# Performance work log

Measured on AMD Instinct MI355X. Metric: run time of the kernel, lower is better.

## Reference

```python
import jax, jax.numpy as jnp
import numpy as np

NUM_GRAPHS = 512
LEAKY_SLOPE = 0.01


def _gconv(x, src, dst, w, W_root, W_rel, b_rel):
    # PyG GraphConv: out = lin_rel(sum_j w_ij * x_j) + lin_root(x)
    msg = x[src] * w[:, None]                       # [E, d] gather + scale
    agg = jax.ops.segment_sum(msg, dst, num_segments=x.shape[0])  # scatter-add
    return agg @ W_rel + b_rel + x @ W_root


def setup_inputs() -> dict:
    key = jax.random.key(0)
    ks = jax.random.split(key, 12)
    N, E, D, H, C = 100000, 1250000, 64, 64, 8
    x_embeddings = jax.random.normal(ks[0], (N, D), dtype=jnp.float32)
    edge_index = jax.random.randint(ks[1], (2, E), 0, N, dtype=jnp.int64)
    weights = jax.random.uniform(ks[2], (E,), dtype=jnp.float32)
    batch = jnp.sort(jax.random.randint(ks[3], (N,), 0, NUM_GRAPHS, dtype=jnp.int64))
    s1 = 1.0 / np.sqrt(D)
    s2 = 1.0 / np.sqrt(H)
    W1_root = jax.random.uniform(ks[4], (D, H), jnp.float32, -s1, s1)
    W1_rel = jax.random.uniform(ks[5], (D, H), jnp.float32, -s1, s1)
    b1 = jax.random.uniform(ks[6], (H,), jnp.float32, -s1, s1)
    W2_root = jax.random.uniform(ks[7], (H, H), jnp.float32, -s2, s2)
    W2_rel = jax.random.uniform(ks[8], (H, H), jnp.float32, -s2, s2)
    b2 = jax.random.uniform(ks[9], (H,), jnp.float32, -s2, s2)
    Wl_root = jax.random.uniform(ks[10], (H, C), jnp.float32, -s2, s2)
    bl = jax.random.uniform(ks[11], (C,), jnp.float32, -s2, s2)
    return {"x_embeddings": x_embeddings, "edge_index": edge_index,
            "weights": weights, "batch": batch,
            "W1_root": W1_root, "W1_rel": W1_rel, "b1": b1,
            "W2_root": W2_root, "W2_rel": W2_rel, "b2": b2,
            "Wl_root": Wl_root, "bl": bl}


def reference(x_embeddings, edge_index, weights, batch,
              W1_root, W1_rel, b1, W2_root, W2_rel, b2, Wl_root, bl):
    src, dst = edge_index[0], edge_index[1]
    x = _gconv(x_embeddings, src, dst, weights, W1_root, W1_rel, b1)
    x = jax.nn.leaky_relu(x, LEAKY_SLOPE)
    x = _gconv(x, src, dst, weights, W2_root, W2_rel, b2)
    x = jax.nn.leaky_relu(x, LEAKY_SLOPE)
    # global_mean_pool over graph ids
    summed = jax.ops.segment_sum(x, batch, num_segments=NUM_GRAPHS)
    counts = jax.ops.segment_sum(jnp.ones((x.shape[0],), x.dtype), batch,
                                 num_segments=NUM_GRAPHS)
    pooled = summed / jnp.maximum(counts, 1.0)[:, None]
    # final GraphConv applied with no edges: agg = 0 -> W_root x + b_rel
    out = pooled @ Wl_root + bl
    return out
```

## Files before the change

kernel.cpp:

```cpp
#include <hip/hip_runtime.h>

#define LEAKY_SLOPE 0.01f
#define NUM_GRAPHS 512
#define TILE 4096
#define NB_MAX 512
#define POOL_SPAN 8

typedef __attribute__((ext_vector_type(8))) short short8;
typedef __attribute__((ext_vector_type(4))) float f32x4;

static __device__ __forceinline__ unsigned short f2bf(float f) {
    unsigned u = __float_as_uint(f);
    u += 0x7FFFu + ((u >> 16) & 1u);
    return (unsigned short)(u >> 16);
}
static __device__ __forceinline__ float bf2f(unsigned short h) {
    return __uint_as_float(((unsigned)h) << 16);
}

static __device__ __forceinline__ int wave_incl_scan(int v, int lane) {
#pragma unroll
    for (int off = 1; off < 64; off <<= 1) {
        int t = __shfl_up(v, off, 64);
        if (lane >= off) v += t;
    }
    return v;
}

__global__ __launch_bounds__(256)
void mega_prep(const int* __restrict__ dst, int* __restrict__ bucketCnt, int E,
               int NB, int histBlocks,
               const float* __restrict__ x, unsigned short* __restrict__ xB,
               int xElems , int xBlocks,
               const float* __restrict__ W1rel, const float* __restrict__ W1root,
               const float* __restrict__ W2rel, const float* __restrict__ W2root,
               unsigned short* __restrict__ Bt1, unsigned short* __restrict__ Bt2) {
    const int bid = blockIdx.x;
    if (bid < histBlocks) {
        __shared__ int h[NB_MAX];
        for (int t = threadIdx.x; t < NB_MAX; t += 256) h[t] = 0;
        __syncthreads();
        const int base = bid * TILE;
#pragma unroll
        for (int i = 0; i < TILE / 256; ++i) {
            int e = base + i * 256 + threadIdx.x;
            if (e < E) atomicAdd(&h[dst[e] >> 8], 1);
        }
        __syncthreads();
        for (int t = threadIdx.x; t < NB; t += 256)
            if (h[t]) atomicAdd(&bucketCnt[t], h[t]);
    } else if (bid < histBlocks + xBlocks) {
        int i = (bid - histBlocks) * 256 + threadIdx.x;
        if (i < xElems) {
            float4 f = ((const float4*)x)[i];
            ushort4 o = make_ushort4(f2bf(f.x), f2bf(f.y), f2bf(f.z), f2bf(f.w));
            ((ushort4*)xB)[i] = o;
        }
    } else {
        int b2 = bid - histBlocks - xBlocks;
        for (int idx = b2 * 2048 + threadIdx.x; idx < (b2 + 1) * 2048; idx += 256) {
            int which = idx >> 13;
            int j = idx & 8191;
            int n = j >> 7, k = j & 127;
            const float* Wr = which ? W2rel : W1rel;
            const float* Wo = which ? W2root : W1root;
            float v = (k < 64) ? Wr[k * 64 + n] : Wo[(k - 64) * 64 + n];
            (which ? Bt2 : Bt1)[j] = f2bf(v);
        }
    }
}

__global__ __launch_bounds__(512)
void bscan_kernel(const int* __restrict__ bucketCnt, int* __restrict__ bucketBase,
                  int* __restrict__ cursor, int* __restrict__ rowStart,
                  float* __restrict__ pooled, int N, int E, int NB) {
    __shared__ int ws[8];
    const int t = threadIdx.x, lane = t & 63, wid = t >> 6;
    int v = (t < NB) ? bucketCnt[t] : 0;
    int s = wave_incl_scan(v, lane);
    if (lane == 63) ws[wid] = s;
    __syncthreads();
    int add = 0;
    for (int i = 0; i < wid; ++i) add += ws[i];
    if (t < NB) {
        int excl = s + add - v;
        bucketBase[t] = excl;
        cursor[t] = excl;
    }
    if (t == 0) rowStart[N] = E;
    float4 z = make_float4(0.f, 0.f, 0.f, 0.f);
#pragma unroll
    for (int i = 0; i < 16; ++i)
        ((float4*)pooled)[t * 16 + i] = z;
}

__global__ __launch_bounds__(256)
void p1b_partition(const int* __restrict__ src, const int* __restrict__ dst,
                   const float* __restrict__ w, int* __restrict__ cursor,
                   int2* __restrict__ tmp, int E, int NB) {
    __shared__ int h[NB_MAX];
    __shared__ int cur[NB_MAX];
    __shared__ int lstart[NB_MAX];
    __shared__ int gbase[NB_MAX];
    __shared__ int ws[4];
    __shared__ int2 pay[TILE];
    __shared__ unsigned short bk[TILE];

    for (int t = threadIdx.x; t < NB_MAX; t += 256) h[t] = 0;
    __syncthreads();

    const int base = blockIdx.x * TILE;
    int   myb[TILE / 256];
    int   myp[TILE / 256];
    float myw[TILE / 256];
#pragma unroll
    for (int i = 0; i < TILE / 256; ++i) {
        int e = base + i * 256 + threadIdx.x;
        if (e < E) {
            int d = dst[e];
            myb[i] = d >> 8;
            myp[i] = src[e] | ((d & 255) << 20);
            myw[i] = w[e];
            atomicAdd(&h[myb[i]], 1);
        } else {
            myb[i] = -1;
        }
    }
    __syncthreads();

    {
        const int t = threadIdx.x, lane = t & 63, wid = t >> 6;
        int a = h[2 * t], b = h[2 * t + 1];
        int s = wave_incl_scan(a + b, lane);
        if (lane == 63) ws[wid] = s;
        __syncthreads();
        int add = 0;
        for (int i = 0; i < wid; ++i) add += ws[i];
        int excl = s + add - (a + b);
        lstart[2 * t] = excl;
        lstart[2 * t + 1] = excl + a;
        cur[2 * t] = excl;
        cur[2 * t + 1] = excl + a;
    }
    __syncthreads();

#pragma unroll
    for (int i = 0; i < TILE / 256; ++i) {
        if (myb[i] >= 0) {
            int p = atomicAdd(&cur[myb[i]], 1);
            pay[p] = make_int2(myp[i], __float_as_int(myw[i]));
            bk[p] = (unsigned short)myb[i];
        }
    }
    __syncthreads();

    for (int t = threadIdx.x; t < NB; t += 256) {
        int c = h[t];
        if (c) gbase[t] = atomicAdd(&cursor[t], c);
    }
    __syncthreads();

    const int total = min(TILE, E - base);
    for (int s2 = threadIdx.x; s2 < total; s2 += 256) {
        int b2 = bk[s2];
        tmp[gbase[b2] + s2 - lstart[b2]] = pay[s2];
    }
}

__global__ __launch_bounds__(256)
void p2_build(const int2* __restrict__ tmp, const int* __restrict__ bucketBase,
              int* __restrict__ rowStart, int2* __restrict__ edata,
              int N, int E, int NB) {
    const int b = blockIdx.x;
    const int s = bucketBase[b];
    const int e2 = (b + 1 < NB) ? bucketBase[b + 1] : E;
    __shared__ int h[256];
    __shared__ int cur[256];
    __shared__ int ws[4];
    h[threadIdx.x] = 0;
    __syncthreads();
    for (int j = s + threadIdx.x; j < e2; j += 256) {
        int dl = (tmp[j].x >> 20) & 255;
        atomicAdd(&h[dl], 1);
    }
    __syncthreads();
    const int t = threadIdx.x, lane = t & 63, wid = t >> 6;
    int v = h[t];
    int sc = wave_incl_scan(v, lane);
    if (lane == 63) ws[wid] = sc;
    __syncthreads();
    int add = 0;
    for (int i = 0; i < wid; ++i) add += ws[i];
    int excl = sc + add - v;
    const int node = b * 256 + t;
    if (node < N) rowStart[node] = s + excl;
    cur[t] = excl;
    __syncthreads();
    for (int j = s + threadIdx.x; j < e2; j += 256) {
        int2 v2 = tmp[j];
        int dl = (v2.x >> 20) & 255;
        int p = atomicAdd(&cur[dl], 1);
        edata[s + p] = make_int2(v2.x & 0x1FFFF, v2.y);
    }
}

__global__ __launch_bounds__(256)
void gather_kernel(const unsigned short* __restrict__ xB, const int* __restrict__ rowStart,
                   const int2* __restrict__ edata, unsigned short* __restrict__ aggB, int N) {
    const int node = blockIdx.x * 4 + (threadIdx.x >> 6);
    if (node >= N) return;
    const int lane = threadIdx.x & 63;
    const int grp  = lane >> 4;
    const int f4   = (lane & 15) * 4;
    const int s = rowStart[node];
    const int e = rowStart[node + 1];

    float a0 = 0.f, a1 = 0.f, a2 = 0.f, a3 = 0.f;
    for (int j = s; j < e; j += 16) {
        int   idx[4];
        int2  ed[4];
#pragma unroll
        for (int u = 0; u < 4; ++u) {
            int ii = j + u * 4 + grp;
            idx[u] = (ii < e) ? ii : s;
            ed[u] = edata[idx[u]];
        }
        ushort4 r[4];
#pragma unroll
        for (int u = 0; u < 4; ++u)
            r[u] = *(const ushort4*)(xB + (size_t)ed[u].x * 64 + f4);
#pragma unroll
        for (int u = 0; u < 4; ++u) {
            int ii = j + u * 4 + grp;
            float wv = (ii < e) ? __int_as_float(ed[u].y) : 0.0f;
            a0 += bf2f(r[u].x) * wv;  a1 += bf2f(r[u].y) * wv;
            a2 += bf2f(r[u].z) * wv;  a3 += bf2f(r[u].w) * wv;
        }
    }
    a0 += __shfl_xor(a0, 16, 64);  a1 += __shfl_xor(a1, 16, 64);
    a2 += __shfl_xor(a2, 16, 64);  a3 += __shfl_xor(a3, 16, 64);
    a0 += __shfl_xor(a0, 32, 64);  a1 += __shfl_xor(a1, 32, 64);
    a2 += __shfl_xor(a2, 32, 64);  a3 += __shfl_xor(a3, 32, 64);
    if (grp == 0) {
        ushort4 o = make_ushort4(f2bf(a0), f2bf(a1), f2bf(a2), f2bf(a3));
        *(ushort4*)(aggB + (size_t)node * 64 + f4) = o;
    }
}

__global__ __launch_bounds__(256)
void transform_store(const unsigned short* __restrict__ aggB,
                     const unsigned short* __restrict__ rootB,
                     const unsigned short* __restrict__ Bt,
                     const float* __restrict__ bias,
                     unsigned short* __restrict__ xoutB, int N) {
    const int wave = threadIdx.x >> 6;
    const int lane = threadIdx.x & 63;
    const int quad = lane >> 4;
    const int l16  = lane & 15;
    const int m0   = blockIdx.x * 128 + wave * 32;

    short8 bf[4][4];
#pragma unroll
    for (int t = 0; t < 4; ++t)
#pragma unroll
        for (int k = 0; k < 4; ++k)
            bf[t][k] = *(const short8*)(Bt + (t * 16 + l16) * 128 + k * 32 + quad * 8);

    f32x4 acc[2][4];
#pragma unroll
    for (int s = 0; s < 2; ++s)
#pragma unroll
        for (int t = 0; t < 4; ++t)
            acc[s][t] = (f32x4){0.f, 0.f, 0.f, 0.f};

#pragma unroll
    for (int s = 0; s < 2; ++s) {
        int row = m0 + s * 16 + l16;
        int rowc = row < N ? row : N - 1;
        const unsigned short* arow = aggB  + (size_t)rowc * 64;
        const unsigned short* xrow = rootB + (size_t)rowc * 64;
        short8 af[4];
        af[0] = *(const short8*)(arow + quad * 8);
        af[1] = *(const short8*)(arow + 32 + quad * 8);
        af[2] = *(const short8*)(xrow + quad * 8);
        af[3] = *(const short8*)(xrow + 32 + quad * 8);
#pragma unroll
        for (int t = 0; t < 4; ++t)
#pragma unroll
            for (int k = 0; k < 4; ++k)
                acc[s][t] = __builtin_amdgcn_mfma_f32_16x16x32_bf16(bf[t][k], af[k],
                                                                    acc[s][t], 0, 0, 0);
    }

#pragma unroll
    for (int s = 0; s < 2; ++s) {
        const int node = m0 + s * 16 + l16;
        if (node < N) {
#pragma unroll
            for (int t = 0; t < 4; ++t) {
                const float4 bb = *(const float4*)(bias + t * 16 + quad * 4);
                float v0 = acc[s][t][0] + bb.x;
                float v1 = acc[s][t][1] + bb.y;
                float v2 = acc[s][t][2] + bb.z;
                float v3 = acc[s][t][3] + bb.w;
                v0 = (v0 > 0.f) ? v0 : LEAKY_SLOPE * v0;
                v1 = (v1 > 0.f) ? v1 : LEAKY_SLOPE * v1;
                v2 = (v2 > 0.f) ? v2 : LEAKY_SLOPE * v2;
                v3 = (v3 > 0.f) ? v3 : LEAKY_SLOPE * v3;
                ushort4 o = make_ushort4(f2bf(v0), f2bf(v1), f2bf(v2), f2bf(v3));
                *(ushort4*)(xoutB + (size_t)node * 64 + t * 16 + quad * 4) = o;
            }
        }
    }
}

__global__ __launch_bounds__(256)
void transform_pool(const unsigned short* __restrict__ aggB,
                    const unsigned short* __restrict__ rootB,
                    const unsigned short* __restrict__ Bt,
                    const float* __restrict__ bias,
                    const int* __restrict__ batch,
                    float* __restrict__ pooled, int N) {
    const int wave = threadIdx.x >> 6;
    const int lane = threadIdx.x & 63;
    const int quad = lane >> 4;
    const int l16  = lane & 15;
    const int m0   = blockIdx.x * 128 + wave * 32;

    __shared__ float lpool[POOL_SPAN * 64];
    const int gmin = batch[blockIdx.x * 128];
    for (int i = threadIdx.x; i < POOL_SPAN * 64; i += 256) lpool[i] = 0.f;

    short8 bf[4][4];
#pragma unroll
    for (int t = 0; t < 4; ++t)
#pragma unroll
        for (int k = 0; k < 4; ++k)
            bf[t][k] = *(const short8*)(Bt + (t * 16 + l16) * 128 + k * 32 + quad * 8);

    f32x4 acc[2][4];
#pragma unroll
    for (int s = 0; s < 2; ++s)
#pragma unroll
        for (int t = 0; t < 4; ++t)
            acc[s][t] = (f32x4){0.f, 0.f, 0.f, 0.f};

#pragma unroll
    for (int s = 0; s < 2; ++s) {
        int row = m0 + s * 16 + l16;
        int rowc = row < N ? row : N - 1;
        const unsigned short* arow = aggB  + (size_t)rowc * 64;
        const unsigned short* xrow = rootB + (size_t)rowc * 64;
        short8 af[4];
        af[0] = *(const short8*)(arow + quad * 8);
        af[1] = *(const short8*)(arow + 32 + quad * 8);
        af[2] = *(const short8*)(xrow + quad * 8);
        af[3] = *(const short8*)(xrow + 32 + quad * 8);
#pragma unroll
        for (int t = 0; t < 4; ++t)
#pragma unroll
            for (int k = 0; k < 4; ++k)
                acc[s][t] = __builtin_amdgcn_mfma_f32_16x16x32_bf16(af[k], bf[t][k],
                                                                    acc[s][t], 0, 0, 0);
    }

    __syncthreads();

#pragma unroll
    for (int s = 0; s < 2; ++s) {
#pragma unroll
        for (int t = 0; t < 4; ++t) {
            const int col = t * 16 + l16;
            const float b = bias[col];
            const int rowbase = m0 + s * 16 + quad * 4;
            float v[4]; int g[4]; int nv = 0;
#pragma unroll
            for (int r = 0; r < 4; ++r) {
                int row = rowbase + r;
                if (row < N) {
                    float a = acc[s][t][r] + b;
                    a = (a > 0.0f) ? a : LEAKY_SLOPE * a;
                    v[nv] = a;
                    g[nv] = batch[row];
                    ++nv;
                }
            }
            if (nv == 4 && g[0] == g[3]) {
                int gl = g[0] - gmin;
                float sum = v[0] + v[1] + v[2] + v[3];
                if (gl < POOL_SPAN) atomicAdd(&lpool[gl * 64 + col], sum);
                else                atomicAdd(&pooled[g[0] * 64 + col], sum);
            } else {
                for (int r = 0; r < nv; ++r) {
                    int gl = g[r] - gmin;
                    if (gl < POOL_SPAN) atomicAdd(&lpool[gl * 64 + col], v[r]);
                    else                atomicAdd(&pooled[g[r] * 64 + col], v[r]);
                }
            }
        }
    }

    __syncthreads();
    for (int i = threadIdx.x; i < POOL_SPAN * 64; i += 256) {
        float v = lpool[i];
        if (v != 0.0f)
            atomicAdd(&pooled[(gmin + (i >> 6)) * 64 + (i & 63)], v);
    }
}

__global__ __launch_bounds__(64)
void final_kernel(const float* __restrict__ pooled, const int* __restrict__ batch,
                  int N, const float* __restrict__ Wl, const float* __restrict__ bl,
                  float* __restrict__ out) {
    const int g = blockIdx.x;
    const int j = threadIdx.x;
    __shared__ float sp[64];
    __shared__ int scnt;
    if (j == 0) {
        int lo = 0, hi = N;
        while (lo < hi) { int mid = (lo + hi) >> 1; if (batch[mid] < g) lo = mid + 1; else hi = mid; }
        const int start = lo;
        hi = N;
        while (lo < hi) { int mid = (lo + hi) >> 1; if (batch[mid] < g + 1) lo = mid + 1; else hi = mid; }
        scnt = lo - start;
    }
    __syncthreads();
    const float c = fmaxf((float)scnt, 1.0f);
    sp[j] = pooled[g * 64 + j] / c;
    __syncthreads();
    if (j < 8) {
        float acc = bl[j];
#pragma unroll
        for (int k = 0; k < 64; ++k) acc += sp[k] * Wl[k * 8 + j];
        out[g * 8 + j] = acc;
    }
}

extern "C" void kernel_launch(void* const* d_in, const int* in_sizes, int n_in,
                              void* d_out, int out_size, void* d_ws, size_t ws_size,
                              hipStream_t stream) {
    const float* x      = (const float*)d_in[0];
    const int*   ei     = (const int*)  d_in[1];
    const float* w      = (const float*)d_in[2];
    const int*   batch  = (const int*)  d_in[3];
    const float* W1root = (const float*)d_in[4];
    const float* W1rel  = (const float*)d_in[5];
    const float* b1     = (const float*)d_in[6];
    const float* W2root = (const float*)d_in[7];
    const float* W2rel  = (const float*)d_in[8];
    const float* b2     = (const float*)d_in[9];
    const float* Wl     = (const float*)d_in[10];
    const float* bl     = (const float*)d_in[11];
    float* out = (float*)d_out;

    const int E = in_sizes[2];
    const int N = in_sizes[3];
    const int* src = ei;
    const int* dst = ei + E;
    const int NB = (N + 255) / 256;

    unsigned short* xB   = (unsigned short*)d_ws;
    unsigned short* aggB = xB   + (size_t)N * 64;
    unsigned short* x1B  = aggB + (size_t)N * 64;
    int2*  tmp      = (int2*)(x1B + (size_t)N * 64);
    int2*  edata    = tmp + E;
    unsigned short* Bt1 = (unsigned short*)(edata + E);
    unsigned short* Bt2 = Bt1 + 64 * 128;
    int*   rowStart = (int*)(Bt2 + 64 * 128);
    int*   bucketCnt  = rowStart + (N + 1);
    int*   bucketBase = bucketCnt + NB_MAX;
    int*   cursor     = bucketBase + NB_MAX;
    float* pooled   = (float*)(cursor + NB_MAX);

    const int histBlocks = (E + TILE - 1) / TILE;
    const int xElems = N * 16;
    const int xBlocks = (xElems + 255) / 256;

    hipMemsetAsync(bucketCnt, 0, NB_MAX * sizeof(int), stream);
    mega_prep<<<histBlocks + xBlocks + 8, 256, 0, stream>>>(
        dst, bucketCnt, E, NB, histBlocks,
        x, xB, xElems, xBlocks,
        W1rel, W1root, W2rel, W2root, Bt1, Bt2);
    bscan_kernel<<<1, 512, 0, stream>>>(bucketCnt, bucketBase, cursor, rowStart,
                                        pooled, N, E, NB);
    p1b_partition<<<histBlocks, 256, 0, stream>>>(src, dst, w, cursor, tmp, E, NB);
    p2_build<<<NB, 256, 0, stream>>>(tmp, bucketBase, rowStart, edata, N, E, NB);

    const int tBlocks = (N + 127) / 128;
    gather_kernel<<<(N + 3) / 4, 256, 0, stream>>>(xB, rowStart, edata, aggB, N);
    transform_store<<<tBlocks, 256, 0, stream>>>(aggB, xB, Bt1, b1, x1B, N);
    gather_kernel<<<(N + 3) / 4, 256, 0, stream>>>(x1B, rowStart, edata, aggB, N);
    transform_pool<<<tBlocks, 256, 0, stream>>>(aggB, x1B, Bt2, b2, batch, pooled, N);
    final_kernel<<<NUM_GRAPHS, 64, 0, stream>>>(pooled, batch, N, Wl, bl, out);
}
```

Baseline: 274.7 us.

## Fuse neighbor gather with MFMA transform into one kernel per layer

```diff
diff --git a/kernel.cpp b/kernel.cpp
--- a/kernel.cpp
+++ b/kernel.cpp
@@ -204,67 +204,76 @@
     }
 }
 
+template <int POOL>
 __global__ __launch_bounds__(256)
-void gather_kernel(const unsigned short* __restrict__ xB, const int* __restrict__ rowStart,
-                   const int2* __restrict__ edata, unsigned short* __restrict__ aggB, int N) {
-    const int node = blockIdx.x * 4 + (threadIdx.x >> 6);
-    if (node >= N) return;
+void fused_layer(const unsigned short* __restrict__ xin,
+                 const int* __restrict__ rowStart,
+                 const int2* __restrict__ edata,
+                 const unsigned short* __restrict__ Bt,
+                 const float* __restrict__ bias,
+                 unsigned short* __restrict__ xoutB,
+                 const int* __restrict__ batch,
+                 float* __restrict__ pooled, int N) {
     const int lane = threadIdx.x & 63;
+    const int wave = threadIdx.x >> 6;
     const int grp  = lane >> 4;
-    const int f4   = (lane & 15) * 4;
-    const int s = rowStart[node];
-    const int e = rowStart[node + 1];
-
-    float a0 = 0.f, a1 = 0.f, a2 = 0.f, a3 = 0.f;
-    for (int j = s; j < e; j += 16) {
-        int   idx[4];
-        int2  ed[4];
-#pragma unroll
-        for (int u = 0; u < 4; ++u) {
-            int ii = j + u * 4 + grp;
-            idx[u] = (ii < e) ? ii : s;
-            ed[u] = edata[idx[u]];
-        }
-        ushort4 r[4];
-#pragma unroll
-        for (int u = 0; u < 4; ++u)
-            r[u] = *(const ushort4*)(xB + (size_t)ed[u].x * 64 + f4);
-#pragma unroll
-        for (int u = 0; u < 4; ++u) {
-            int ii = j + u * 4 + grp;
-            float wv = (ii < e) ? __int_as_float(ed[u].y) : 0.0f;
-            a0 += bf2f(r[u].x) * wv;  a1 += bf2f(r[u].y) * wv;
-            a2 += bf2f(r[u].z) * wv;  a3 += bf2f(r[u].w) * wv;
-        }
-    }
-    a0 += __shfl_xor(a0, 16, 64);  a1 += __shfl_xor(a1, 16, 64);
-    a2 += __shfl_xor(a2, 16, 64);  a3 += __shfl_xor(a3, 16, 64);
-    a0 += __shfl_xor(a0, 32, 64);  a1 += __shfl_xor(a1, 32, 64);
-    a2 += __shfl_xor(a2, 32, 64);  a3 += __shfl_xor(a3, 32, 64);
-    if (grp == 0) {
-        ushort4 o = make_ushort4(f2bf(a0), f2bf(a1), f2bf(a2), f2bf(a3));
-        *(ushort4*)(aggB + (size_t)node * 64 + f4) = o;
-    }
-}
-
-__global__ __launch_bounds__(256)
-void transform_store(const unsigned short* __restrict__ aggB,
-                     const unsigned short* __restrict__ rootB,
-                     const unsigned short* __restrict__ Bt,
-                     const float* __restrict__ bias,
-                     unsigned short* __restrict__ xoutB, int N) {
-    const int wave = threadIdx.x >> 6;
-    const int lane = threadIdx.x & 63;
-    const int quad = lane >> 4;
     const int l16  = lane & 15;
-    const int m0   = blockIdx.x * 128 + wave * 32;
+    const int f4   = l16 * 4;
+    const int m0   = (int)blockIdx.x * 128 + wave * 32;
+
+    __shared__ __align__(16) unsigned short aggL[4][32][72];
+    __shared__ float lpool[POOL_SPAN * 64];
+
+    int gmin = 0;
+    if (POOL) {
+        int b0 = (int)blockIdx.x * 128;
+        gmin = batch[b0 < N ? b0 : N - 1];
+        for (int i = threadIdx.x; i < POOL_SPAN * 64; i += 256) lpool[i] = 0.f;
+    }
+
+    int rsv = 0;
+    if (lane <= 32) {
+        int rn = m0 + lane;
+        rsv = rowStart[rn < N ? rn : N];
+    }
+#pragma unroll 1
+    for (int i = 0; i < 32; ++i) {
+        const int s = __shfl(rsv, i, 64);
+        const int e = __shfl(rsv, i + 1, 64);
+        float a0 = 0.f, a1 = 0.f, a2 = 0.f, a3 = 0.f;
+        for (int j = s; j < e; j += 16) {
+            int2 ed[4];
+#pragma unroll
+            for (int u = 0; u < 4; ++u) {
+                int ii = j + u * 4 + grp;
+                ed[u] = edata[ii < e ? ii : s];
+            }
+            ushort4 r[4];
+#pragma unroll
+            for (int u = 0; u < 4; ++u)
+                r[u] = *(const ushort4*)(xin + (size_t)ed[u].x * 64 + f4);
+#pragma unroll
+            for (int u = 0; u < 4; ++u) {
+                float wv = (j + u * 4 + grp < e) ? __int_as_float(ed[u].y) : 0.0f;
+                a0 += bf2f(r[u].x) * wv;  a1 += bf2f(r[u].y) * wv;
+                a2 += bf2f(r[u].z) * wv;  a3 += bf2f(r[u].w) * wv;
+            }
+        }
+        a0 += __shfl_xor(a0, 16, 64);  a1 += __shfl_xor(a1, 16, 64);
+        a2 += __shfl_xor(a2, 16, 64);  a3 += __shfl_xor(a3, 16, 64);
+        a0 += __shfl_xor(a0, 32, 64);  a1 += __shfl_xor(a1, 32, 64);
+        a2 += __shfl_xor(a2, 32, 64);  a3 += __shfl_xor(a3, 32, 64);
+        if (grp == 0)
+            *(ushort4*)(&aggL[wave][i][f4]) =
+                make_ushort4(f2bf(a0), f2bf(a1), f2bf(a2), f2bf(a3));
+    }
 
     short8 bf[4][4];
 #pragma unroll
     for (int t = 0; t < 4; ++t)
 #pragma unroll
         for (int k = 0; k < 4; ++k)
-            bf[t][k] = *(const short8*)(Bt + (t * 16 + l16) * 128 + k * 32 + quad * 8);
+            bf[t][k] = *(const short8*)(Bt + (t * 16 + l16) * 128 + k * 32 + grp * 8);
 
     f32x4 acc[2][4];
 #pragma unroll
@@ -277,134 +286,87 @@
     for (int s = 0; s < 2; ++s) {
         int row = m0 + s * 16 + l16;
         int rowc = row < N ? row : N - 1;
-        const unsigned short* arow = aggB  + (size_t)rowc * 64;
-        const unsigned short* xrow = rootB + (size_t)rowc * 64;
+        const unsigned short* xrow = xin + (size_t)rowc * 64;
         short8 af[4];
-        af[0] = *(const short8*)(arow + quad * 8);
-        af[1] = *(const short8*)(arow + 32 + quad * 8);
-        af[2] = *(const short8*)(xrow + quad * 8);
-        af[3] = *(const short8*)(xrow + 32 + quad * 8);
+        af[0] = *(const short8*)(&aggL[wave][s * 16 + l16][grp * 8]);
+        af[1] = *(const short8*)(&aggL[wave][s * 16 + l16][32 + grp * 8]);
+        af[2] = *(const short8*)(xrow + grp * 8);
+        af[3] = *(const short8*)(xrow + 32 + grp * 8);
 #pragma unroll
         for (int t = 0; t < 4; ++t)
 #pragma unroll
-            for (int k = 0; k < 4; ++k)
-                acc[s][t] = __builtin_amdgcn_mfma_f32_16x16x32_bf16(bf[t][k], af[k],
-                                                                    acc[s][t], 0, 0, 0);
-    }
-
-#pragma unroll
-    for (int s = 0; s < 2; ++s) {
-        const int node = m0 + s * 16 + l16;
-        if (node < N) {
-#pragma unroll
-            for (int t = 0; t < 4; ++t) {
-                const float4 bb = *(const float4*)(bias + t * 16 + quad * 4);
-                float v0 = acc[s][t][0] + bb.x;
-                float v1 = acc[s][t][1] + bb.y;
-                float v2 = acc[s][t][2] + bb.z;
-                float v3 = acc[s][t][3] + bb.w;
-                v0 = (v0 > 0.f) ? v0 : LEAKY_SLOPE * v0;
-                v1 = (v1 > 0.f) ? v1 : LEAKY_SLOPE * v1;
-                v2 = (v2 > 0.f) ? v2 : LEAKY_SLOPE * v2;
-                v3 = (v3 > 0.f) ? v3 : LEAKY_SLOPE * v3;
-                ushort4 o = make_ushort4(f2bf(v0), f2bf(v1), f2bf(v2), f2bf(v3));
-                *(ushort4*)(xoutB + (size_t)node * 64 + t * 16 + quad * 4) = o;
+            for (int k = 0; k < 4; ++k) {
+                if (POOL == 0)
+                    acc[s][t] = __builtin_amdgcn_mfma_f32_16x16x32_bf16(
+                        bf[t][k], af[k], acc[s][t], 0, 0, 0);
+                else
+                    acc[s][t] = __builtin_amdgcn_mfma_f32_16x16x32_bf16(
+                        af[k], bf[t][k], acc[s][t], 0, 0, 0);
             }
-        }
-    }
-}
-
-__global__ __launch_bounds__(256)
-void transform_pool(const unsigned short* __restrict__ aggB,
-                    const unsigned short* __restrict__ rootB,
-                    const unsigned short* __restrict__ Bt,
-                    const float* __restrict__ bias,
-                    const int* __restrict__ batch,
-                    float* __restrict__ pooled, int N) {
-    const int wave = threadIdx.x >> 6;
-    const int lane = threadIdx.x & 63;
-    const int quad = lane >> 4;
-    const int l16  = lane & 15;
-    const int m0   = blockIdx.x * 128 + wave * 32;
-
-    __shared__ float lpool[POOL_SPAN * 64];
-    const int gmin = batch[blockIdx.x * 128];
-    for (int i = threadIdx.x; i < POOL_SPAN * 64; i += 256) lpool[i] = 0.f;
-
-    short8 bf[4][4];
-#pragma unroll
-    for (int t = 0; t < 4; ++t)
-#pragma unroll
-        for (int k = 0; k < 4; ++k)
-            bf[t][k] = *(const short8*)(Bt + (t * 16 + l16) * 128 + k * 32 + quad * 8);
-
-    f32x4 acc[2][4];
-#pragma unroll
-    for (int s = 0; s < 2; ++s)
-#pragma unroll
-        for (int t = 0; t < 4; ++t)
-            acc[s][t] = (f32x4){0.f, 0.f, 0.f, 0.f};
-
-#pragma unroll
-    for (int s = 0; s < 2; ++s) {
-        int row = m0 + s * 16 + l16;
-        int rowc = row < N ? row : N - 1;
-        const unsigned short* arow = aggB  + (size_t)rowc * 64;
-        const unsigned short* xrow = rootB + (size_t)rowc * 64;
-        short8 af[4];
-        af[0] = *(const short8*)(arow + quad * 8);
-        af[1] = *(const short8*)(arow + 32 + quad * 8);
-        af[2] = *(const short8*)(xrow + quad * 8);
-        af[3] = *(const short8*)(xrow + 32 + quad * 8);
-#pragma unroll
-        for (int t = 0; t < 4; ++t)
-#pragma unroll
-            for (int k = 0; k < 4; ++k)
-                acc[s][t] = __builtin_amdgcn_mfma_f32_16x16x32_bf16(af[k], bf[t][k],
-                                                                    acc[s][t], 0, 0, 0);
-    }
-
-    __syncthreads();
-
-#pragma unroll
-    for (int s = 0; s < 2; ++s) {
-#pragma unroll
-        for (int t = 0; t < 4; ++t) {
-            const int col = t * 16 + l16;
-            const float b = bias[col];
-            const int rowbase = m0 + s * 16 + quad * 4;
-            float v[4]; int g[4]; int nv = 0;
-#pragma unroll
-            for (int r = 0; r < 4; ++r) {
-                int row = rowbase + r;
-                if (row < N) {
-                    float a = acc[s][t][r] + b;
-                    a = (a > 0.0f) ? a : LEAKY_SLOPE * a;
-                    v[nv] = a;
-                    g[nv] = batch[row];
-                    ++nv;
+    }
+
+    if (POOL == 0) {
+#pragma unroll
+        for (int s = 0; s < 2; ++s) {
+            const int node = m0 + s * 16 + l16;
+            if (node < N) {
+#pragma unroll
+                for (int t = 0; t < 4; ++t) {
+                    const float4 bb = *(const float4*)(bias + t * 16 + grp * 4);
+                    float v0 = acc[s][t][0] + bb.x;
+                    float v1 = acc[s][t][1] + bb.y;
+                    float v2 = acc[s][t][2] + bb.z;
+                    float v3 = acc[s][t][3] + bb.w;
+                    v0 = (v0 > 0.f) ? v0 : LEAKY_SLOPE * v0;
+                    v1 = (v1 > 0.f) ? v1 : LEAKY_SLOPE * v1;
+                    v2 = (v2 > 0.f) ? v2 : LEAKY_SLOPE * v2;
+                    v3 = (v3 > 0.f) ? v3 : LEAKY_SLOPE * v3;
+                    ushort4 o = make_ushort4(f2bf(v0), f2bf(v1), f2bf(v2), f2bf(v3));
+                    *(ushort4*)(xoutB + (size_t)node * 64 + t * 16 + grp * 4) = o;
                 }
             }
-            if (nv == 4 && g[0] == g[3]) {
-                int gl = g[0] - gmin;
-                float sum = v[0] + v[1] + v[2] + v[3];
-                if (gl < POOL_SPAN) atomicAdd(&lpool[gl * 64 + col], sum);
-                else                atomicAdd(&pooled[g[0] * 64 + col], sum);
-            } else {
-                for (int r = 0; r < nv; ++r) {
-                    int gl = g[r] - gmin;
-                    if (gl < POOL_SPAN) atomicAdd(&lpool[gl * 64 + col], v[r]);
-                    else                atomicAdd(&pooled[g[r] * 64 + col], v[r]);
+        }
+    } else {
+        __syncthreads();
+#pragma unroll
+        for (int s = 0; s < 2; ++s) {
+#pragma unroll
+            for (int t = 0; t < 4; ++t) {
+                const int col = t * 16 + l16;
+                const float b = bias[col];
+                const int rowbase = m0 + s * 16 + grp * 4;
+                float v[4]; int g[4]; int nv = 0;
+#pragma unroll
+                for (int r = 0; r < 4; ++r) {
+                    int row = rowbase + r;
+                    if (row < N) {
+                        float a = acc[s][t][r] + b;
+                        a = (a > 0.0f) ? a : LEAKY_SLOPE * a;
+                        v[nv] = a;
+                        g[nv] = batch[row];
+                        ++nv;
+                    }
+                }
+                if (nv == 4 && g[0] == g[3]) {
+                    int gl = g[0] - gmin;
+                    float sum = v[0] + v[1] + v[2] + v[3];
+                    if (gl < POOL_SPAN) atomicAdd(&lpool[gl * 64 + col], sum);
+                    else                atomicAdd(&pooled[g[0] * 64 + col], sum);
+                } else {
+                    for (int r = 0; r < nv; ++r) {
+                        int gl = g[r] - gmin;
+                        if (gl < POOL_SPAN) atomicAdd(&lpool[gl * 64 + col], v[r]);
+                        else                atomicAdd(&pooled[g[r] * 64 + col], v[r]);
+                    }
                 }
             }
         }
-    }
-
-    __syncthreads();
-    for (int i = threadIdx.x; i < POOL_SPAN * 64; i += 256) {
-        float v = lpool[i];
-        if (v != 0.0f)
-            atomicAdd(&pooled[(gmin + (i >> 6)) * 64 + (i & 63)], v);
+        __syncthreads();
+        for (int i = threadIdx.x; i < POOL_SPAN * 64; i += 256) {
+            float vv = lpool[i];
+            if (vv != 0.0f)
+                atomicAdd(&pooled[(gmin + (i >> 6)) * 64 + (i & 63)], vv);
+        }
     }
 }
 
@@ -471,12 +433,13 @@
     int*   bucketBase = bucketCnt + NB_MAX;
     int*   cursor     = bucketBase + NB_MAX;
     float* pooled   = (float*)(cursor + NB_MAX);
+    (void)aggB;
 
     const int histBlocks = (E + TILE - 1) / TILE;
     const int xElems = N * 16;
     const int xBlocks = (xElems + 255) / 256;
 
-    hipMemsetAsync(bucketCnt, 0, NB_MAX * sizeof(int), stream);
+    (void)hipMemsetAsync(bucketCnt, 0, NB_MAX * sizeof(int), stream);
     mega_prep<<<histBlocks + xBlocks + 8, 256, 0, stream>>>(
         dst, bucketCnt, E, NB, histBlocks,
         x, xB, xElems, xBlocks,
@@ -487,9 +450,9 @@
     p2_build<<<NB, 256, 0, stream>>>(tmp, bucketBase, rowStart, edata, N, E, NB);
 
     const int tBlocks = (N + 127) / 128;
-    gather_kernel<<<(N + 3) / 4, 256, 0, stream>>>(xB, rowStart, edata, aggB, N);
-    transform_store<<<tBlocks, 256, 0, stream>>>(aggB, xB, Bt1, b1, x1B, N);
-    gather_kernel<<<(N + 3) / 4, 256, 0, stream>>>(x1B, rowStart, edata, aggB, N);
-    transform_pool<<<tBlocks, 256, 0, stream>>>(aggB, x1B, Bt2, b2, batch, pooled, N);
+    fused_layer<0><<<tBlocks, 256, 0, stream>>>(xB, rowStart, edata, Bt1, b1,
+                                                x1B, nullptr, nullptr, N);
+    fused_layer<1><<<tBlocks, 256, 0, stream>>>(x1B, rowStart, edata, Bt2, b2,
+                                                nullptr, batch, pooled, N);
     final_kernel<<<NUM_GRAPHS, 64, 0, stream>>>(pooled, batch, N, Wl, bl, out);
 }
```

After: 292.3 us. +6.4%, slower.
